# Optimization experiments

Hardware: AMD Instinct MI355X
Metric: run time of the kernel (lower is better)

Reference implementation:

```python
import jax, jax.numpy as jnp
import numpy as np

B, H, W, C = 32, 56, 56, 512
HEADS, WS, SS = 16, 7, 3
N = WS * WS            # window area = 49
HD = C // HEADS        # head dim = 32
HID = 4 * C            # mlp hidden = 2048
nWh, nWw = H // WS, W // WS
nW = nWh * nWw


def _rel_pos_index():
    # static (N, N) int index into relative_position_bias_table
    coords = np.stack(np.meshgrid(np.arange(WS), np.arange(WS), indexing='ij'))  # (2, WS, WS)
    cf = coords.reshape(2, -1)                       # (2, N)
    rel = (cf[:, :, None] - cf[:, None, :]).transpose(1, 2, 0).copy()  # (N, N, 2)
    rel[:, :, 0] += WS - 1
    rel[:, :, 1] += WS - 1
    rel[:, :, 0] *= 2 * WS - 1
    return rel.sum(-1)  # (N, N)


def _attn_mask():
    # static shifted-window attention mask, (nW, N, N) with 0 / -100
    img = np.zeros((H, W))
    cnt = 0
    for h0, h1 in ((0, H - WS), (H - WS, H - SS), (H - SS, H)):
        for w0, w1 in ((0, W - WS), (W - WS, W - SS), (W - SS, W)):
            img[h0:h1, w0:w1] = cnt
            cnt += 1
    mw = img.reshape(nWh, WS, nWw, WS).transpose(0, 2, 1, 3).reshape(-1, N)  # (nW, N)
    diff = mw[:, None, :] - mw[:, :, None]
    return np.where(diff != 0, -100.0, 0.0).astype(np.float32)

_REL_IDX = _rel_pos_index()
_MASK = _attn_mask()


def _ln(x, g, b, eps=1e-5):
    mu = x.mean(-1, keepdims=True)
    var = ((x - mu) ** 2).mean(-1, keepdims=True)
    return (x - mu) * jax.lax.rsqrt(var + eps) * g + b


def setup_inputs() -> dict:
    key = jax.random.key(0)
    ks = jax.random.split(key, 8)
    s = lambda k, shape: jax.random.normal(k, shape, jnp.float32) * 0.02
    return {
        'x': jax.random.normal(ks[0], (B, H, W, C), jnp.float32),
        'norm1_g': jnp.ones((C,), jnp.float32), 'norm1_b': jnp.zeros((C,), jnp.float32),
        'qkv_w': s(ks[1], (3 * C, C)), 'qkv_b': jnp.zeros((3 * C,), jnp.float32),
        'rel_pos_table': s(ks[2], ((2 * WS - 1) ** 2, HEADS)),
        'proj_w': s(ks[3], (C, C)), 'proj_b': jnp.zeros((C,), jnp.float32),
        'norm2_g': jnp.ones((C,), jnp.float32), 'norm2_b': jnp.zeros((C,), jnp.float32),
        'fc1_w': s(ks[4], (HID, C)), 'fc1_b': jnp.zeros((HID,), jnp.float32),
        'fc2_w': s(ks[5], (C, HID)), 'fc2_b': jnp.zeros((C,), jnp.float32),
    }


def reference(x, norm1_g, norm1_b, qkv_w, qkv_b, rel_pos_table, proj_w, proj_b,
              norm2_g, norm2_b, fc1_w, fc1_b, fc2_w, fc2_b):
    shortcut = x
    y = _ln(x, norm1_g, norm1_b)
    # cyclic shift
    y = jnp.roll(y, (-SS, -SS), axis=(1, 2))
    # window partition -> (B*nW, N, C)
    yw = y.reshape(B, nWh, WS, nWw, WS, C).transpose(0, 1, 3, 2, 4, 5).reshape(B * nW, N, C)
    # qkv projection
    qkv = yw @ qkv_w.T + qkv_b
    qkv = qkv.reshape(B * nW, N, 3, HEADS, HD).transpose(2, 0, 3, 1, 4)
    q, k, v = qkv[0], qkv[1], qkv[2]              # each (B*nW, HEADS, N, HD)
    scale = HD ** -0.5
    attn = jnp.einsum('bhqd,bhkd->bhqk', q * scale, k)  # (B*nW, HEADS, N, N)
    # relative position bias gather
    bias = rel_pos_table[jnp.asarray(_REL_IDX.reshape(-1))].reshape(N, N, HEADS)
    attn = attn + bias.transpose(2, 0, 1)[None]
    # shifted-window mask
    attn = attn.reshape(B, nW, HEADS, N, N) + jnp.asarray(_MASK)[None, :, None]
    attn = jax.nn.softmax(attn.reshape(B * nW, HEADS, N, N), axis=-1)
    o = jnp.einsum('bhqk,bhkd->bhqd', attn, v)
    o = o.transpose(0, 2, 1, 3).reshape(B * nW, N, C)
    o = o @ proj_w.T + proj_b
    # window reverse + reverse shift
    o = o.reshape(B, nWh, nWw, WS, WS, C).transpose(0, 1, 3, 2, 4, 5).reshape(B, H, W, C)
    o = jnp.roll(o, (SS, SS), axis=(1, 2))
    x = shortcut + o
    # MLP
    h = _ln(x, norm2_g, norm2_b)
    h = jax.nn.gelu(h @ fc1_w.T + fc1_b, approximate=False)
    h = h @ fc2_w.T + fc2_b
    return x + h
```

## Files before the change

kernel.cpp:

```cpp
#include <hip/hip_runtime.h>

#define Bb   32
#define Hh   56
#define Ww_  56
#define Cc   512
#define HEADS 16
#define WS   7
#define SS   3
#define Nn   49
#define HD   32
#define HID  2048
#define NWIN 2048
#define NTOK 100352

typedef __attribute__((ext_vector_type(4))) float f32x4;
typedef __attribute__((ext_vector_type(8))) short bf16x8;

#define AS1 __attribute__((address_space(1)))
#define AS3 __attribute__((address_space(3)))

__device__ __forceinline__ ushort f2bf(float x) {
  union { float f; unsigned u; } un; un.f = x;
  unsigned u = un.u;
  return (ushort)((u + 0x7fffu + ((u >> 16) & 1u)) >> 16);
}

__global__ void cvtw_kern(const float* __restrict__ s, ushort* __restrict__ d, int n) {
  int i = blockIdx.x * 256 + threadIdx.x;
  if (i < n) d[i] = f2bf(s[i]);
}

__global__ void zero_vpad_kern(ushort* __restrict__ vb) {
  int i = blockIdx.x * 256 + threadIdx.x;
  if (i < NWIN * 16 * 32) {
    ushort* p = vb + (size_t)i * 64 + 49;
    #pragma unroll
    for (int e = 0; e < 15; ++e) p[e] = 0;
  }
}

__global__ void prep_bias_kern(const float* __restrict__ table, float* __restrict__ be) {
  int idx = blockIdx.x * 256 + threadIdx.x;
  int h = idx >> 12, q = (idx >> 6) & 63, k = idx & 63;
  float v = -1e30f;
  if (q < Nn && k < Nn) {
    int qi = q / 7, qj = q - qi * 7;
    int ki = k / 7, kj = k - ki * 7;
    v = table[((qi - ki + 6) * 13 + (qj - kj + 6)) * HEADS + h];
  }
  be[idx] = v;
}

template<int MODE>
__global__ __launch_bounds__(256) void ln_kern(const float* __restrict__ x,
    const float* __restrict__ g, const float* __restrict__ bsh,
    ushort* __restrict__ out)
{
  int row  = blockIdx.x * 4 + (threadIdx.x >> 6);
  int lane = threadIdx.x & 63;
  const float* src;
  if (MODE == 0) {
    unsigned w = (unsigned)row / 49u, n = (unsigned)row - w * 49u;
    unsigned bb = w >> 6, wi = w & 63;
    unsigned wh = wi >> 3, ww = wi & 7;
    unsigned i = n / 7u, j = n - i * 7u;
    unsigned sr = wh * 7 + i + SS; if (sr >= Hh) sr -= Hh;
    unsigned sc = ww * 7 + j + SS; if (sc >= Ww_) sc -= Ww_;
    src = x + ((size_t)(bb * Hh + sr) * Ww_ + sc) * Cc;
  } else {
    src = x + (size_t)row * Cc;
  }
  int c = lane * 8;
  f32x4 v0 = *(const f32x4*)(src + c);
  f32x4 v1 = *(const f32x4*)(src + c + 4);
  float s = 0.f, s2 = 0.f;
  #pragma unroll
  for (int e = 0; e < 4; ++e) { s += v0[e]; s2 += v0[e]*v0[e]; s += v1[e]; s2 += v1[e]*v1[e]; }
  #pragma unroll
  for (int off = 32; off; off >>= 1) { s += __shfl_xor(s, off); s2 += __shfl_xor(s2, off); }
  float mu = s * (1.f / 512.f);
  float rstd = rsqrtf(s2 * (1.f / 512.f) - mu * mu + 1e-5f);
  bf16x8 r;
  #pragma unroll
  for (int e = 0; e < 8; ++e) {
    float xv = (e < 4) ? v0[e] : v1[e - 4];
    r[e] = (short)f2bf((xv - mu) * rstd * g[c + e] + bsh[c + e]);
  }
  *(bf16x8*)(out + (size_t)row * Cc + c) = r;
}

template<int EPI>
__global__ __launch_bounds__(256, 2) void gemm_kern(
    const ushort* __restrict__ A, const ushort* __restrict__ Bw,
    const float* __restrict__ bias, int M, int N, int K,
    void* __restrict__ outp, const float* __restrict__ resid,
    ushort* __restrict__ qb, ushort* __restrict__ kb, ushort* __restrict__ vb)
{
  __shared__ ushort As[128 * 64];
  __shared__ ushort Bs[128 * 64];
  const int tid = threadIdx.x;
  const int wave = tid >> 6, lane = tid & 63;
  const int l15 = lane & 15, lhi = lane >> 4;
  const int sw7 = l15 & 7;

  int gx = gridDim.x;
  int nwg = gx * gridDim.y;
  int orig = blockIdx.y * gx + blockIdx.x;
  int cpx = nwg >> 3;
  int wg = (orig & 7) * cpx + (orig >> 3);
  int bx = wg % gx, by = wg / gx;
  const int brow = by * 128, bcol = bx * 128;

  const int wr = (wave >> 1) * 64, wc = (wave & 1) * 64;

  const int srow = lane >> 3;
  const int schk = ((lane & 7) ^ srow) * 8;
  const ushort* aG = A  + (size_t)(brow + srow) * K + schk;
  const ushort* bG = Bw + (size_t)(bcol + srow) * K + schk;

  f32x4 acc[4][4];
  #pragma unroll
  for (int m = 0; m < 4; ++m)
    #pragma unroll
    for (int n = 0; n < 4; ++n)
      acc[m][n] = (f32x4){0.f, 0.f, 0.f, 0.f};

  for (int k0 = 0; k0 < K; k0 += 64) {
    if (k0) __syncthreads();
    #pragma unroll
    for (int s = 0; s < 4; ++s) {
      int rg = (s * 4 + wave) * 8;
      __builtin_amdgcn_global_load_lds(
        (const AS1 void*)(aG + (size_t)rg * K + k0),
        (AS3 void*)&As[rg * 64], 16, 0, 0);
      __builtin_amdgcn_global_load_lds(
        (const AS1 void*)(bG + (size_t)rg * K + k0),
        (AS3 void*)&Bs[rg * 64], 16, 0, 0);
    }
    __syncthreads();
    #pragma unroll
    for (int kk = 0; kk < 2; ++kk) {
      bf16x8 af[4], bfr[4];
      #pragma unroll
      for (int m = 0; m < 4; ++m) {
        af[m]  = *(const bf16x8*)&As[(wr + m * 16 + l15) * 64 + (((kk * 4 + lhi) ^ sw7)) * 8];
        bfr[m] = *(const bf16x8*)&Bs[(wc + m * 16 + l15) * 64 + (((kk * 4 + lhi) ^ sw7)) * 8];
      }
      #pragma unroll
      for (int m = 0; m < 4; ++m)
        #pragma unroll
        for (int n = 0; n < 4; ++n)
          acc[m][n] = __builtin_amdgcn_mfma_f32_16x16x32_bf16(af[m], bfr[n], acc[m][n], 0, 0, 0);
    }
  }

  float bv[4];
  #pragma unroll
  for (int n = 0; n < 4; ++n) bv[n] = bias[bcol + wc + n * 16 + l15];
  #pragma unroll
  for (int m = 0; m < 4; ++m) {
    int rbase = brow + wr + m * 16 + lhi * 4;
    #pragma unroll
    for (int n = 0; n < 4; ++n) {
      int cc = bcol + wc + n * 16 + l15;
      #pragma unroll
      for (int j = 0; j < 4; ++j) {
        unsigned r = (unsigned)(rbase + j);
        float v = acc[m][n][j] + bv[n];
        if (EPI == 0) {
          unsigned w = r / 49u, nn = r - w * 49u;
          int part = cc >> 9, head = (cc >> 5) & 15, d = cc & 31;
          size_t wh = (size_t)(w * HEADS + head);
          ushort bvs = f2bf(v);
          if (part == 0)      qb[(wh * 64 + nn) * 32 + d] = bvs;
          else if (part == 1) kb[(wh * 64 + nn) * 32 + d] = bvs;
          else                vb[(wh * 32 + d) * 64 + nn] = bvs;
        } else if (EPI == 1) {
          float u2 = v * (1.5957691216f + 0.0713548162f * v * v);
          float gl = __fdividef(v, 1.0f + __expf(-u2));
          ((ushort*)outp)[(size_t)r * N + cc] = f2bf(gl);
        } else if (EPI == 2) {
          unsigned w = r / 49u, nn = r - w * 49u;
          unsigned bb = w >> 6, wi = w & 63;
          unsigned wh = wi >> 3, ww = wi & 7;
          unsigned ii = nn / 7u, jj = nn - ii * 7u;
          unsigned dr = wh * 7 + ii + SS; if (dr >= Hh) dr -= Hh;
          unsigned dc = ww * 7 + jj + SS; if (dc >= Ww_) dc -= Ww_;
          size_t p = ((size_t)bb * Hh + dr) * Ww_ + dc;
          ((float*)outp)[p * Cc + cc] = resid[p * Cc + cc] + v;
        } else {
          float* o = (float*)outp;
          size_t idx = (size_t)r * Cc + cc;
          o[idx] = o[idx] + v;
        }
      }
    }
  }
}

__global__ __launch_bounds__(256) void attn_kern(
    const ushort* __restrict__ qb, const ushort* __restrict__ kb,
    const ushort* __restrict__ vb, const float* __restrict__ be_g,
    ushort* __restrict__ o_win)
{
  __shared__ ushort P[4][4096];
  const int wv = threadIdx.x >> 6, lane = threadIdx.x & 63;
  const int l15 = lane & 15, lhi = lane >> 4;
  const int w = blockIdx.x;
  const int wi = w & 63, whh = wi >> 3, www = wi & 7;
  ushort* Pl = P[wv];

  int krg[4];
  #pragma unroll
  for (int n = 0; n < 4; ++n) {
    int key = n * 16 + l15;
    int rg = -1;
    if (key < Nn) {
      int ki = key / 7, kj = key - ki * 7;
      int rr = whh * 7 + ki, cc = www * 7 + kj;
      rg = (rr < 49 ? 0 : (rr < 53 ? 1 : 2)) * 3 + (cc < 49 ? 0 : (cc < 53 ? 1 : 2));
    }
    krg[n] = rg;
  }
  int qrg[4][4];
  #pragma unroll
  for (int m = 0; m < 4; ++m)
    #pragma unroll
    for (int j = 0; j < 4; ++j) {
      int q = m * 16 + lhi * 4 + j;
      int rg = -2;
      if (q < Nn) {
        int qi = q / 7, qj = q - qi * 7;
        int rr = whh * 7 + qi, cc = www * 7 + qj;
        rg = (rr < 49 ? 0 : (rr < 53 ? 1 : 2)) * 3 + (cc < 49 ? 0 : (cc < 53 ? 1 : 2));
      }
      qrg[m][j] = rg;
    }

  for (int head = wv; head < HEADS; head += 4) {
    const ushort* qp = qb + (size_t)(w * HEADS + head) * 2048;
    const ushort* kp = kb + (size_t)(w * HEADS + head) * 2048;
    const ushort* vp = vb + (size_t)(w * HEADS + head) * 2048;
    bf16x8 qf[4], kf[4];
    #pragma unroll
    for (int m = 0; m < 4; ++m) {
      qf[m] = *(const bf16x8*)(qp + (m * 16 + l15) * 32 + lhi * 8);
      kf[m] = *(const bf16x8*)(kp + (m * 16 + l15) * 32 + lhi * 8);
    }
    f32x4 sa[4][4];
    #pragma unroll
    for (int m = 0; m < 4; ++m)
      #pragma unroll
      for (int n = 0; n < 4; ++n)
        sa[m][n] = __builtin_amdgcn_mfma_f32_16x16x32_bf16(qf[m], kf[n],
                     (f32x4){0.f, 0.f, 0.f, 0.f}, 0, 0, 0);

    const float* be = be_g + head * 4096;
    #pragma unroll
    for (int m = 0; m < 4; ++m)
      #pragma unroll
      for (int n = 0; n < 4; ++n)
        #pragma unroll
        for (int j = 0; j < 4; ++j) {
          int q = m * 16 + lhi * 4 + j, key = n * 16 + l15;
          float v;
          if (qrg[m][j] >= 0 && krg[n] >= 0) {
            v = sa[m][n][j] * 0.17677669529663687f + be[q * 64 + key];
            if (qrg[m][j] != krg[n]) v -= 100.0f;
          } else v = -1e30f;
          sa[m][n][j] = v;
        }
    #pragma unroll
    for (int m = 0; m < 4; ++m)
      #pragma unroll
      for (int j = 0; j < 4; ++j) {
        float mx = fmaxf(fmaxf(sa[m][0][j], sa[m][1][j]), fmaxf(sa[m][2][j], sa[m][3][j]));
        #pragma unroll
        for (int off = 8; off; off >>= 1) mx = fmaxf(mx, __shfl_xor(mx, off));
        float sum = 0.f;
        #pragma unroll
        for (int n = 0; n < 4; ++n) { float p = __expf(sa[m][n][j] - mx); sa[m][n][j] = p; sum += p; }
        #pragma unroll
        for (int off = 8; off; off >>= 1) sum += __shfl_xor(sum, off);
        float is = 1.0f / sum;
        #pragma unroll
        for (int n = 0; n < 4; ++n) sa[m][n][j] *= is;
      }
    #pragma unroll
    for (int m = 0; m < 4; ++m)
      #pragma unroll
      for (int n = 0; n < 4; ++n)
        #pragma unroll
        for (int j = 0; j < 4; ++j) {
          int q = m * 16 + lhi * 4 + j, key = n * 16 + l15;
          int bo = (q * 128 + key * 2) ^ ((q & 7) << 4);
          *(ushort*)((char*)Pl + bo) = f2bf(sa[m][n][j]);
        }
    __syncthreads();
    bf16x8 vf[2][2];
    #pragma unroll
    for (int nt = 0; nt < 2; ++nt)
      #pragma unroll
      for (int kt = 0; kt < 2; ++kt)
        vf[nt][kt] = *(const bf16x8*)(vp + (nt * 16 + l15) * 64 + kt * 32 + lhi * 8);
    f32x4 oa[4][2];
    #pragma unroll
    for (int m = 0; m < 4; ++m)
      #pragma unroll
      for (int nt = 0; nt < 2; ++nt)
        oa[m][nt] = (f32x4){0.f, 0.f, 0.f, 0.f};
    #pragma unroll
    for (int m = 0; m < 4; ++m) {
      int row = m * 16 + l15;
      #pragma unroll
      for (int kt = 0; kt < 2; ++kt) {
        int bo = (row * 128 + kt * 64 + lhi * 16) ^ ((row & 7) << 4);
        bf16x8 pa = *(const bf16x8*)((char*)Pl + bo);
        #pragma unroll
        for (int nt = 0; nt < 2; ++nt)
          oa[m][nt] = __builtin_amdgcn_mfma_f32_16x16x32_bf16(pa, vf[nt][kt], oa[m][nt], 0, 0, 0);
      }
    }
    #pragma unroll
    for (int m = 0; m < 4; ++m) {
      int q0 = m * 16 + lhi * 4;
      #pragma unroll
      for (int nt = 0; nt < 2; ++nt) {
        int d = nt * 16 + l15;
        #pragma unroll
        for (int j = 0; j < 4; ++j) {
          int q = q0 + j;
          if (q < Nn)
            o_win[((size_t)w * Nn + q) * Cc + head * HD + d] = f2bf(oa[m][nt][j]);
        }
      }
    }
    __syncthreads();
  }
}

extern "C" void kernel_launch(void* const* d_in, const int* in_sizes, int n_in,
                              void* d_out, int out_size, void* d_ws, size_t ws_size,
                              hipStream_t stream) {
  const float* x      = (const float*)d_in[0];
  const float* n1g    = (const float*)d_in[1];
  const float* n1b    = (const float*)d_in[2];
  const float* qkv_w  = (const float*)d_in[3];
  const float* qkv_b  = (const float*)d_in[4];
  const float* relt   = (const float*)d_in[5];
  const float* proj_w = (const float*)d_in[6];
  const float* proj_b = (const float*)d_in[7];
  const float* n2g    = (const float*)d_in[8];
  const float* n2b    = (const float*)d_in[9];
  const float* fc1_w  = (const float*)d_in[10];
  const float* fc1_b  = (const float*)d_in[11];
  const float* fc2_w  = (const float*)d_in[12];
  const float* fc2_b  = (const float*)d_in[13];

  char* ws = (char*)d_ws;
  ushort* wq = (ushort*)ws; ws += (size_t)1536 * 512 * 2;
  ushort* wp = (ushort*)ws; ws += (size_t)512 * 512 * 2;
  ushort* w1 = (ushort*)ws; ws += (size_t)2048 * 512 * 2;
  ushort* w2 = (ushort*)ws; ws += (size_t)512 * 2048 * 2;
  float*  be = (float*)ws;  ws += (size_t)16 * 64 * 64 * 4;
  ushort* buf1 = (ushort*)ws; ws += (size_t)NTOK * 2048 * 2;
  ushort* qbuf = (ushort*)ws; ws += (size_t)NWIN * 16 * 64 * 32 * 2;
  ushort* kbuf = (ushort*)ws; ws += (size_t)NWIN * 16 * 64 * 32 * 2;
  ushort* vbuf = (ushort*)ws; ws += (size_t)NWIN * 16 * 64 * 32 * 2;
  ushort* yw = buf1;
  ushort* o_win = buf1;
  ushort* h1 = buf1;
  ushort* l2buf = qbuf;
  float* xout = (float*)d_out;

  cvtw_kern<<<(1536 * 512 + 255) / 256, 256, 0, stream>>>(qkv_w, wq, 1536 * 512);
  cvtw_kern<<<(512 * 512 + 255) / 256, 256, 0, stream>>>(proj_w, wp, 512 * 512);
  cvtw_kern<<<(2048 * 512 + 255) / 256, 256, 0, stream>>>(fc1_w, w1, 2048 * 512);
  cvtw_kern<<<(512 * 2048 + 255) / 256, 256, 0, stream>>>(fc2_w, w2, 512 * 2048);
  zero_vpad_kern<<<(NWIN * 16 * 32 + 255) / 256, 256, 0, stream>>>(vbuf);
  prep_bias_kern<<<65536 / 256, 256, 0, stream>>>(relt, be);

  ln_kern<0><<<NTOK / 4, 256, 0, stream>>>(x, n1g, n1b, yw);
  gemm_kern<0><<<dim3(12, 784), 256, 0, stream>>>(yw, wq, qkv_b, NTOK, 1536, 512,
                                                  nullptr, nullptr, qbuf, kbuf, vbuf);
  attn_kern<<<NWIN, 256, 0, stream>>>(qbuf, kbuf, vbuf, be, o_win);
  gemm_kern<2><<<dim3(4, 784), 256, 0, stream>>>(o_win, wp, proj_b, NTOK, 512, 512,
                                                 xout, x, nullptr, nullptr, nullptr);
  ln_kern<1><<<NTOK / 4, 256, 0, stream>>>(xout, n2g, n2b, l2buf);
  gemm_kern<1><<<dim3(16, 784), 256, 0, stream>>>(l2buf, w1, fc1_b, NTOK, 2048, 512,
                                                  h1, nullptr, nullptr, nullptr, nullptr);
  gemm_kern<3><<<dim3(4, 784), 256, 0, stream>>>(h1, w2, fc2_b, NTOK, 512, 2048,
                                                 xout, xout, nullptr, nullptr, nullptr);
}
```

Baseline: 1.532 ms.

## Split attention grid across heads and vectorize bias loads with fused softmax

The attention kernel now launches one block per window and group of four heads, so each wave handles exactly one head. This removes the per-block head loop and its two block-wide barriers, and exposes four times more blocks for occupancy. The bias table is pre-permuted so each lane fetches its four key biases with a single float4 load, and masking is fused with the per-row softmax. The separate kernel that zeroed V padding is dropped, which relies on the padded V entries being finite: their probabilities are zero, but any NaN or Inf left in the workspace would propagate.

New measurement: 1.341 ms. 12.5% less time.

```diff
diff --git a/kernel.cpp b/kernel.cpp
--- a/kernel.cpp
+++ b/kernel.cpp
@@ -30,25 +30,18 @@
   if (i < n) d[i] = f2bf(s[i]);
 }
 
-__global__ void zero_vpad_kern(ushort* __restrict__ vb) {
-  int i = blockIdx.x * 256 + threadIdx.x;
-  if (i < NWIN * 16 * 32) {
-    ushort* p = vb + (size_t)i * 64 + 49;
-    #pragma unroll
-    for (int e = 0; e < 15; ++e) p[e] = 0;
-  }
-}
-
-__global__ void prep_bias_kern(const float* __restrict__ table, float* __restrict__ be) {
+__global__ void prep_bias_kern(const float* __restrict__ table, float* __restrict__ be2) {
   int idx = blockIdx.x * 256 + threadIdx.x;
-  int h = idx >> 12, q = (idx >> 6) & 63, k = idx & 63;
-  float v = -1e30f;
-  if (q < Nn && k < Nn) {
+  int h = idx >> 12, q = (idx >> 6) & 63, t = idx & 63;
+  int l15 = t >> 2, n = t & 3;
+  int key = n * 16 + l15;
+  float v = 0.f;
+  if (q < Nn && key < Nn) {
     int qi = q / 7, qj = q - qi * 7;
-    int ki = k / 7, kj = k - ki * 7;
+    int ki = key / 7, kj = key - ki * 7;
     v = table[((qi - ki + 6) * 13 + (qj - kj + 6)) * HEADS + h];
   }
-  be[idx] = v;
+  be2[idx] = v;
 }
 
 template<int MODE>
@@ -200,13 +193,14 @@
 
 __global__ __launch_bounds__(256) void attn_kern(
     const ushort* __restrict__ qb, const ushort* __restrict__ kb,
-    const ushort* __restrict__ vb, const float* __restrict__ be_g,
+    const ushort* __restrict__ vb, const float* __restrict__ be2,
     ushort* __restrict__ o_win)
 {
   __shared__ ushort P[4][4096];
   const int wv = threadIdx.x >> 6, lane = threadIdx.x & 63;
   const int l15 = lane & 15, lhi = lane >> 4;
   const int w = blockIdx.x;
+  const int head = blockIdx.y * 4 + wv;
   const int wi = w & 63, whh = wi >> 3, www = wi & 7;
   ushort* Pl = P[wv];
 
@@ -237,105 +231,96 @@
       qrg[m][j] = rg;
     }
 
-  for (int head = wv; head < HEADS; head += 4) {
-    const ushort* qp = qb + (size_t)(w * HEADS + head) * 2048;
-    const ushort* kp = kb + (size_t)(w * HEADS + head) * 2048;
-    const ushort* vp = vb + (size_t)(w * HEADS + head) * 2048;
-    bf16x8 qf[4], kf[4];
-    #pragma unroll
-    for (int m = 0; m < 4; ++m) {
-      qf[m] = *(const bf16x8*)(qp + (m * 16 + l15) * 32 + lhi * 8);
-      kf[m] = *(const bf16x8*)(kp + (m * 16 + l15) * 32 + lhi * 8);
-    }
-    f32x4 sa[4][4];
-    #pragma unroll
-    for (int m = 0; m < 4; ++m)
-      #pragma unroll
-      for (int n = 0; n < 4; ++n)
-        sa[m][n] = __builtin_amdgcn_mfma_f32_16x16x32_bf16(qf[m], kf[n],
-                     (f32x4){0.f, 0.f, 0.f, 0.f}, 0, 0, 0);
-
-    const float* be = be_g + head * 4096;
-    #pragma unroll
-    for (int m = 0; m < 4; ++m)
-      #pragma unroll
-      for (int n = 0; n < 4; ++n)
-        #pragma unroll
-        for (int j = 0; j < 4; ++j) {
-          int q = m * 16 + lhi * 4 + j, key = n * 16 + l15;
-          float v;
-          if (qrg[m][j] >= 0 && krg[n] >= 0) {
-            v = sa[m][n][j] * 0.17677669529663687f + be[q * 64 + key];
-            if (qrg[m][j] != krg[n]) v -= 100.0f;
-          } else v = -1e30f;
-          sa[m][n][j] = v;
-        }
-    #pragma unroll
-    for (int m = 0; m < 4; ++m)
+  const ushort* qp = qb + (size_t)(w * HEADS + head) * 2048;
+  const ushort* kp = kb + (size_t)(w * HEADS + head) * 2048;
+  const ushort* vp = vb + (size_t)(w * HEADS + head) * 2048;
+  const float*  bep = be2 + head * 4096;
+
+  bf16x8 qf[4], kf[4];
+  #pragma unroll
+  for (int m = 0; m < 4; ++m) {
+    qf[m] = *(const bf16x8*)(qp + (m * 16 + l15) * 32 + lhi * 8);
+    kf[m] = *(const bf16x8*)(kp + (m * 16 + l15) * 32 + lhi * 8);
+  }
+  f32x4 sa[4][4];
+  #pragma unroll
+  for (int m = 0; m < 4; ++m)
+    #pragma unroll
+    for (int n = 0; n < 4; ++n)
+      sa[m][n] = __builtin_amdgcn_mfma_f32_16x16x32_bf16(qf[m], kf[n],
+                   (f32x4){0.f, 0.f, 0.f, 0.f}, 0, 0, 0);
+
+  #pragma unroll
+  for (int m = 0; m < 4; ++m)
+    #pragma unroll
+    for (int j = 0; j < 4; ++j) {
+      int q = m * 16 + lhi * 4 + j;
+      int qr = qrg[m][j];
+      f32x4 bev = *(const f32x4*)(bep + q * 64 + l15 * 4);
+      float vv[4];
+      float mx = -1e30f;
+      #pragma unroll
+      for (int n = 0; n < 4; ++n) {
+        float v;
+        if (qr >= 0 && krg[n] >= 0) {
+          v = sa[m][n][j] * 0.17677669529663687f + bev[n];
+          if (qr != krg[n]) v -= 100.0f;
+        } else v = -1e30f;
+        vv[n] = v;
+        mx = fmaxf(mx, v);
+      }
+      #pragma unroll
+      for (int off = 8; off; off >>= 1) mx = fmaxf(mx, __shfl_xor(mx, off));
+      float sum = 0.f;
+      #pragma unroll
+      for (int n = 0; n < 4; ++n) { float p = __expf(vv[n] - mx); vv[n] = p; sum += p; }
+      #pragma unroll
+      for (int off = 8; off; off >>= 1) sum += __shfl_xor(sum, off);
+      float is = 1.0f / sum;
+      #pragma unroll
+      for (int n = 0; n < 4; ++n) {
+        int bo = (q * 128 + (n * 16 + l15) * 2) ^ ((q & 7) << 4);
+        *(ushort*)((char*)Pl + bo) = f2bf(vv[n] * is);
+      }
+    }
+
+  bf16x8 vf[2][2];
+  #pragma unroll
+  for (int nt = 0; nt < 2; ++nt)
+    #pragma unroll
+    for (int kt = 0; kt < 2; ++kt)
+      vf[nt][kt] = *(const bf16x8*)(vp + (nt * 16 + l15) * 64 + kt * 32 + lhi * 8);
+  f32x4 oa[4][2];
+  #pragma unroll
+  for (int m = 0; m < 4; ++m)
+    #pragma unroll
+    for (int nt = 0; nt < 2; ++nt)
+      oa[m][nt] = (f32x4){0.f, 0.f, 0.f, 0.f};
+  #pragma unroll
+  for (int m = 0; m < 4; ++m) {
+    int row = m * 16 + l15;
+    #pragma unroll
+    for (int kt = 0; kt < 2; ++kt) {
+      int bo = (row * 128 + kt * 64 + lhi * 16) ^ ((row & 7) << 4);
+      bf16x8 pa = *(const bf16x8*)((char*)Pl + bo);
+      #pragma unroll
+      for (int nt = 0; nt < 2; ++nt)
+        oa[m][nt] = __builtin_amdgcn_mfma_f32_16x16x32_bf16(pa, vf[nt][kt], oa[m][nt], 0, 0, 0);
+    }
+  }
+  #pragma unroll
+  for (int m = 0; m < 4; ++m) {
+    int q0 = m * 16 + lhi * 4;
+    #pragma unroll
+    for (int nt = 0; nt < 2; ++nt) {
+      int d = nt * 16 + l15;
       #pragma unroll
       for (int j = 0; j < 4; ++j) {
-        float mx = fmaxf(fmaxf(sa[m][0][j], sa[m][1][j]), fmaxf(sa[m][2][j], sa[m][3][j]));
-        #pragma unroll
-        for (int off = 8; off; off >>= 1) mx = fmaxf(mx, __shfl_xor(mx, off));
-        float sum = 0.f;
-        #pragma unroll
-        for (int n = 0; n < 4; ++n) { float p = __expf(sa[m][n][j] - mx); sa[m][n][j] = p; sum += p; }
-        #pragma unroll
-        for (int off = 8; off; off >>= 1) sum += __shfl_xor(sum, off);
-        float is = 1.0f / sum;
-        #pragma unroll
-        for (int n = 0; n < 4; ++n) sa[m][n][j] *= is;
-      }
-    #pragma unroll
-    for (int m = 0; m < 4; ++m)
-      #pragma unroll
-      for (int n = 0; n < 4; ++n)
-        #pragma unroll
-        for (int j = 0; j < 4; ++j) {
-          int q = m * 16 + lhi * 4 + j, key = n * 16 + l15;
-          int bo = (q * 128 + key * 2) ^ ((q & 7) << 4);
-          *(ushort*)((char*)Pl + bo) = f2bf(sa[m][n][j]);
-        }
-    __syncthreads();
-    bf16x8 vf[2][2];
-    #pragma unroll
-    for (int nt = 0; nt < 2; ++nt)
-      #pragma unroll
-      for (int kt = 0; kt < 2; ++kt)
-        vf[nt][kt] = *(const bf16x8*)(vp + (nt * 16 + l15) * 64 + kt * 32 + lhi * 8);
-    f32x4 oa[4][2];
-    #pragma unroll
-    for (int m = 0; m < 4; ++m)
-      #pragma unroll
-      for (int nt = 0; nt < 2; ++nt)
-        oa[m][nt] = (f32x4){0.f, 0.f, 0.f, 0.f};
-    #pragma unroll
-    for (int m = 0; m < 4; ++m) {
-      int row = m * 16 + l15;
-      #pragma unroll
-      for (int kt = 0; kt < 2; ++kt) {
-        int bo = (row * 128 + kt * 64 + lhi * 16) ^ ((row & 7) << 4);
-        bf16x8 pa = *(const bf16x8*)((char*)Pl + bo);
-        #pragma unroll
-        for (int nt = 0; nt < 2; ++nt)
-          oa[m][nt] = __builtin_amdgcn_mfma_f32_16x16x32_bf16(pa, vf[nt][kt], oa[m][nt], 0, 0, 0);
-      }
-    }
-    #pragma unroll
-    for (int m = 0; m < 4; ++m) {
-      int q0 = m * 16 + lhi * 4;
-      #pragma unroll
-      for (int nt = 0; nt < 2; ++nt) {
-        int d = nt * 16 + l15;
-        #pragma unroll
-        for (int j = 0; j < 4; ++j) {
-          int q = q0 + j;
-          if (q < Nn)
-            o_win[((size_t)w * Nn + q) * Cc + head * HD + d] = f2bf(oa[m][nt][j]);
-        }
-      }
-    }
-    __syncthreads();
+        int q = q0 + j;
+        if (q < Nn)
+          o_win[((size_t)w * Nn + q) * Cc + head * HD + d] = f2bf(oa[m][nt][j]);
+      }
+    }
   }
 }
 
@@ -377,13 +362,12 @@
   cvtw_kern<<<(512 * 512 + 255) / 256, 256, 0, stream>>>(proj_w, wp, 512 * 512);
   cvtw_kern<<<(2048 * 512 + 255) / 256, 256, 0, stream>>>(fc1_w, w1, 2048 * 512);
   cvtw_kern<<<(512 * 2048 + 255) / 256, 256, 0, stream>>>(fc2_w, w2, 512 * 2048);
-  zero_vpad_kern<<<(NWIN * 16 * 32 + 255) / 256, 256, 0, stream>>>(vbuf);
   prep_bias_kern<<<65536 / 256, 256, 0, stream>>>(relt, be);
 
   ln_kern<0><<<NTOK / 4, 256, 0, stream>>>(x, n1g, n1b, yw);
   gemm_kern<0><<<dim3(12, 784), 256, 0, stream>>>(yw, wq, qkv_b, NTOK, 1536, 512,
                                                   nullptr, nullptr, qbuf, kbuf, vbuf);
-  attn_kern<<<NWIN, 256, 0, stream>>>(qbuf, kbuf, vbuf, be, o_win);
+  attn_kern<<<dim3(NWIN, 4), 256, 0, stream>>>(qbuf, kbuf, vbuf, be, o_win);
   gemm_kern<2><<<dim3(4, 784), 256, 0, stream>>>(o_win, wp, proj_b, NTOK, 512, 512,
                                                  xout, x, nullptr, nullptr, nullptr);
   ln_kern<1><<<NTOK / 4, 256, 0, stream>>>(xout, n2g, n2b, l2buf);
```
